# Kernel optimization log

Hardware: AMD Instinct MI355X
Metric: run time of the kernel (lower is better)

The kernel has to match this reference:

```python
import jax, jax.numpy as jnp
import numpy as np

S, B, NS, NC = 128, 64, 128, 8
D, Z, H, HI, NF = 32, 64, 128, 128, 2
N = NS * B
LOG2PI = float(np.log(2.0 * np.pi))
_m_in = np.arange(1, Z + 1)
_m_hid = (np.arange(HI) % (Z - 1)) + 1
MASK1 = jnp.asarray((_m_hid[None, :] >= _m_in[:, None]).astype(np.float32))  # [Z,HI]
MASK2 = jnp.asarray((_m_in[None, :] > _m_hid[:, None]).astype(np.float32))   # [HI,Z]


def setup_inputs() -> dict:
    key = jax.random.key(0)
    ks = jax.random.split(key, 16)
    r = lambda i, shape: jax.random.normal(ks[i], shape, jnp.float32) * 0.1
    return dict(
        input=jax.random.normal(ks[0], (S, B, D), jnp.float32),
        eps=jax.random.normal(ks[1], (S, N, Z), jnp.float32),
        u=jax.random.uniform(ks[2], (S, 3, NC, NS, B), dtype=jnp.float32),
        Wxh=r(3, (D, H)), Wzh=r(4, (Z, H)), bh=jnp.zeros(H, jnp.float32),
        Wg=r(5, (H, Z)), bg=jnp.zeros(Z, jnp.float32),
        Wp=r(6, (H, Z)), bp=jnp.zeros(Z, jnp.float32),
        Wz=r(7, (Z, Z)), bz=jnp.zeros(Z, jnp.float32),
        Wsc=r(8, (Z, Z)), bsc=jnp.zeros(Z, jnp.float32),
        iaf_W1=r(9, (NF, Z, HI)), iaf_b1=jnp.zeros((NF, HI), jnp.float32),
        iaf_Wm=r(10, (NF, HI, Z)), iaf_bm=jnp.zeros((NF, Z), jnp.float32),
        iaf_Ws=r(11, (NF, HI, Z)), iaf_bs=jnp.zeros((NF, Z), jnp.float32),
        We1=r(12, (Z, H)), be1=jnp.zeros(H, jnp.float32),
        We2=r(13, (H, 4 * NC)), be2=jnp.zeros(4 * NC, jnp.float32),
    )


def _forward(input, eps, u, Wxh, Wzh, bh, Wg, bg, Wp, bp, Wz, bz, Wsc, bsc,
             iaf_W1, iaf_b1, iaf_Wm, iaf_bm, iaf_Ws, iaf_bs, We1, be1, We2, be2):
    def step(z_prev, inp):
        x, eps_t, u_t = inp                        # x:[B,D] eps_t:[N,Z] u_t:[3,NC,NS,B]
        xr = jnp.tile(x, (NS, 1))                  # == input[i].repeat(n_samples, 1) -> [N,D]
        # GatedTransition
        h = jax.nn.relu(xr @ Wxh + z_prev @ Wzh + bh)
        gate = jax.nn.sigmoid(h @ Wg + bg)
        prop = h @ Wp + bp
        loc = (1.0 - gate) * (z_prev @ Wz + bz) + gate * prop
        scale = jax.nn.softplus(jax.nn.relu(prop) @ Wsc + bsc) + 1e-3
        # base rsample + log_prob of base sample (eps form)
        z = loc + scale * eps_t
        base_lp = jnp.sum(-0.5 * eps_t * eps_t - jnp.log(scale) - 0.5 * LOG2PI, axis=-1)
        # IAF stack: y = sigma*x + (1-sigma)*mu, cached log_prob = base_lp - sum log sigma
        logdet = jnp.zeros((N,), z.dtype)
        for f in range(NF):
            hh = jax.nn.relu(z @ (iaf_W1[f] * MASK1) + iaf_b1[f])
            mu = hh @ (iaf_Wm[f] * MASK2) + iaf_bm[f]
            sg = jax.nn.sigmoid(hh @ (iaf_Ws[f] * MASK2) + iaf_bs[f] + 1.0)
            z = sg * z + (1.0 - sg) * mu
            logdet = logdet + jnp.sum(jnp.log(sg), axis=-1)
        z_lp = (base_lp - logdet).reshape(NS, B)
        # Emitter -> [N, 4*NC]; .t().view(4,NC,NS,B).split([3,1])
        e = jax.nn.relu(z @ We1 + be1) @ We2 + be2
        et = e.T.reshape(4, NC, NS, B)
        logits, frac = et[:3], jax.nn.sigmoid(et[3:4])
        samp = (u_t < jax.nn.sigmoid(logits)).astype(jnp.float32)  # Bernoulli sample
        x_lp = samp * jax.nn.log_sigmoid(logits) + (1.0 - samp) * jax.nn.log_sigmoid(-logits)
        return z, (samp, frac, x_lp, z_lp)

    z0 = jnp.zeros((N, Z), input.dtype)
    _, (samples, fractions, x_logprobs, z_logprobs) = jax.lax.scan(step, z0, (input, eps, u))
    return samples, fractions, x_logprobs, z_logprobs


def reference(input, eps, u, Wxh, Wzh, bh, Wg, bg, Wp, bp, Wz, bz, Wsc, bsc,
              iaf_W1, iaf_b1, iaf_Wm, iaf_bm, iaf_Ws, iaf_bs, We1, be1, We2, be2):
    return _forward(input, eps, u, Wxh, Wzh, bh, Wg, bg, Wp, bp, Wz, bz, Wsc, bsc,
                    iaf_W1, iaf_b1, iaf_Wm, iaf_bm, iaf_Ws, iaf_bs, We1, be1, We2, be2)
```

## Files before the change

### kernel.cpp

```cpp
#include <hip/hip_runtime.h>


typedef _Float16 f16x8 __attribute__((ext_vector_type(8)));
typedef _Float16 f16x4 __attribute__((ext_vector_type(4)));
typedef float    f32x4 __attribute__((ext_vector_type(4)));
typedef unsigned short u16;

#define MFMA16(a,b,c) __builtin_amdgcn_mfma_f32_16x16x32_f16((a),(b),(c),0,0,0)

namespace {
constexpr int S = 128;
constexpr long FRAC_OFF = 25165824L;
constexpr long XLP_OFF  = 33554432L;
constexpr long ZLP_OFF  = 58720256L;
constexpr float HLOG2PI = 0.91893853320467274f;
constexpr float INVLO   = 1.0f / 2048.0f;

constexpr int C1HI = 0,      C1LO = 12288;
constexpr int GPHI = 24576,  GPLO = 40960;
constexpr int WZHI = 57344,  WZLO = 61440;
constexpr int SCHI = 65536,  SCLO = 69632;
constexpr int W1B  = 73728;
constexpr int MSB  = 106496;
constexpr int E1HI = 172032, E1LO = 180224;
constexpr int E2HI = 188416, E2LO = 192512;
constexpr int XHI  = 196608, XLO  = 458752;
}

__device__ __forceinline__ float sigm(float x)      { return 1.0f / (1.0f + __expf(-x)); }
__device__ __forceinline__ float softplusf_(float x){ return fmaxf(x, 0.f) + __logf(1.f + __expf(-fabsf(x))); }
__device__ __forceinline__ float logsigm(float x)   { return fminf(x, 0.f) - __logf(1.f + __expf(-fabsf(x))); }

__device__ __forceinline__ void split2(float v, _Float16& hi, _Float16& lo) {
    hi = (_Float16)v;
    lo = (_Float16)((v - (float)hi) * 2048.0f);
}

__device__ __forceinline__ f16x8 rdA(const u16* t, int row, int k, int strideEls, int swm) {
    int byte = ((row * strideEls + k) * 2) ^ ((row & swm) << 4);
    return *(const f16x8*)((const char*)t + byte);
}
__device__ __forceinline__ f16x8 ldB(const u16* wa, int base, int col, int K, int koff) {
    return *(const f16x8*)(wa + base + col * K + koff);
}

template<int NKS, int STRIDE, int SWM>
__device__ __forceinline__ void mmDual(const u16* Th, const u16* Tl, int lnc, int kf,
                                       const f16x8 (&wh)[NKS], const f16x8 (&wl)[NKS],
                                       float bias, f32x4& H0, f32x4& L0, f32x4& H1, f32x4& L1)
{
    H0 = (f32x4){bias, bias, bias, bias}; H1 = H0;
    L0 = (f32x4){0.f, 0.f, 0.f, 0.f};     L1 = L0;
#pragma unroll
    for (int ks = 0; ks < NKS; ++ks) {
        int k = ks * 32 + kf;
        f16x8 a0h = rdA(Th, lnc,      k, STRIDE, SWM);
        f16x8 a0l = rdA(Tl, lnc,      k, STRIDE, SWM);
        f16x8 a1h = rdA(Th, 16 + lnc, k, STRIDE, SWM);
        f16x8 a1l = rdA(Tl, 16 + lnc, k, STRIDE, SWM);
        H0 = MFMA16(a0h, wh[ks], H0); L0 = MFMA16(a0h, wl[ks], L0); L0 = MFMA16(a0l, wh[ks], L0);
        H1 = MFMA16(a1h, wh[ks], H1); L1 = MFMA16(a1h, wl[ks], L1); L1 = MFMA16(a1l, wh[ks], L1);
    }
}

template<bool RELU>
__device__ __forceinline__ void stAct(f32x4 H, f32x4 L, int rt, int lng, int col,
                                      u16* th, u16* tl, int strideEls, int swm)
{
#pragma unroll
    for (int q = 0; q < 4; ++q) {
        int row = rt * 16 + lng * 4 + q;
        float v = H[q] + L[q] * INVLO;
        if (RELU) v = fmaxf(v, 0.f);
        _Float16 hi, lo; split2(v, hi, lo);
        int byte = ((row * strideEls + col) * 2) ^ ((row & swm) << 4);
        *(_Float16*)((char*)th + byte) = hi;
        *(_Float16*)((char*)tl + byte) = lo;
    }
}
__device__ __forceinline__ void stScr(f32x4 H, f32x4 L, int rt, int lng, int col,
                                      float* s, int strideEls)
{
#pragma unroll
    for (int q = 0; q < 4; ++q) {
        int row = rt * 16 + lng * 4 + q;
        int byte = ((row * strideEls + col) * 4) ^ ((row & 7) << 4);
        *(float*)((char*)s + byte) = H[q] + L[q] * INVLO;
    }
}
__device__ __forceinline__ f32x4 rdS4(const float* s, int strideEls, int row, int c) {
    int byte = ((row * strideEls + c) * 4) ^ ((row & 7) << 4);
    return *(const f32x4*)((const char*)s + byte);
}
__device__ __forceinline__ float rdS1(const float* s, int strideEls, int row, int c) {
    int byte = ((row * strideEls + c) * 4) ^ ((row & 7) << 4);
    return *(const float*)((const char*)s + byte);
}
__device__ __forceinline__ void wrS4(float* s, int strideEls, int row, int c, f32x4 v) {
    int byte = ((row * strideEls + c) * 4) ^ ((row & 7) << 4);
    *(f32x4*)((char*)s + byte) = v;
}
__device__ __forceinline__ void wrF16x4(u16* t, int strideEls, int row, int c, f16x4 v) {
    int byte = ((row * strideEls + c) * 2) ^ ((row & 7) << 4);
    *(f16x4*)((char*)t + byte) = v;
}
__device__ __forceinline__ f16x4 rdF16x4(const u16* t, int strideEls, int row, int c) {
    int byte = ((row * strideEls + c) * 2) ^ ((row & 7) << 4);
    return *(const f16x4*)((const char*)t + byte);
}

__global__ void prep_kernel(const float* __restrict__ input,
                            const float* __restrict__ Wxh, const float* __restrict__ Wzh,
                            const float* __restrict__ Wg,  const float* __restrict__ Wp,
                            const float* __restrict__ Wz,  const float* __restrict__ Wsc,
                            const float* __restrict__ W1,  const float* __restrict__ Wm,
                            const float* __restrict__ Ws_, const float* __restrict__ We1,
                            const float* __restrict__ We2, u16* __restrict__ wa)
{
    int idx = blockIdx.x * 256 + threadIdx.x;
    if (idx < 98304) {
        int hio = 0, loo = 0; float v = 0.f;
        int i = idx;
        if (i < 12288) {
            int col = i / 96, k = i % 96;
            v = (k < 32) ? Wxh[k * 128 + col] : Wzh[(k - 32) * 128 + col];
            hio = C1HI + i; loo = C1LO + i;
        } else if (i < 28672) { int j = i - 12288;
            int col = j >> 7, k = j & 127;
            v = (col < 64) ? Wg[k * 64 + col] : Wp[k * 64 + col - 64];
            hio = GPHI + j; loo = GPLO + j;
        } else if (i < 32768) { int j = i - 28672;
            int col = j >> 6, k = j & 63; v = Wz[k * 64 + col];
            hio = WZHI + j; loo = WZLO + j;
        } else if (i < 36864) { int j = i - 32768;
            int col = j >> 6, k = j & 63; v = Wsc[k * 64 + col];
            hio = SCHI + j; loo = SCLO + j;
        } else if (i < 53248) { int j = i - 36864;
            int f = j >> 13, jj = j & 8191;
            int col = jj >> 6, k = jj & 63;
            v = W1[(f * 64 + k) * 128 + col] * (((col % 63) >= k) ? 1.f : 0.f);
            hio = W1B + f * 16384 + jj; loo = hio + 8192;
        } else if (i < 86016) { int j = i - 53248;
            int f = j >> 14, jj = j & 16383;
            int col = jj >> 7, k = jj & 127;
            if (col < 64) v = Wm[(f * 128 + k) * 64 + col] * (((k % 63) < col) ? 1.f : 0.f);
            else { int c = col - 64;
                   v = Ws_[(f * 128 + k) * 64 + c]         * (((k % 63) < c)   ? 1.f : 0.f); }
            hio = MSB + f * 32768 + jj; loo = hio + 16384;
        } else if (i < 94208) { int j = i - 86016;
            int col = j >> 6, k = j & 63; v = We1[k * 128 + col];
            hio = E1HI + j; loo = E1LO + j;
        } else { int j = i - 94208;
            int col = j >> 7, k = j & 127; v = We2[k * 32 + col];
            hio = E2HI + j; loo = E2LO + j;
        }
        _Float16 hi, lo; split2(v, hi, lo);
        wa[hio] = __builtin_bit_cast(u16, hi);
        wa[loo] = __builtin_bit_cast(u16, lo);
    } else {
        int j = idx - 98304;
        if (j < 262144) {
            float v = input[j];
            _Float16 hi, lo; split2(v, hi, lo);
            wa[XHI + j] = __builtin_bit_cast(u16, hi);
            wa[XLO + j] = __builtin_bit_cast(u16, lo);
        }
    }
}

__global__ __launch_bounds__(512, 2)
void ssm_mfma_kernel(const float* __restrict__ eps, const float* __restrict__ u,
                     const float* __restrict__ bh,  const float* __restrict__ bg,
                     const float* __restrict__ bp,  const float* __restrict__ bz,
                     const float* __restrict__ bsc, const float* __restrict__ b1,
                     const float* __restrict__ bm,  const float* __restrict__ bs,
                     const float* __restrict__ be1, const float* __restrict__ be2,
                     const u16* __restrict__ wa, float* __restrict__ out)
{
    __shared__ u16 tXh[32 * 32],  tXl[32 * 32];
    __shared__ u16 tZh[32 * 64],  tZl[32 * 64];
    __shared__ u16 tHh[32 * 128], tHl[32 * 128];
    __shared__ u16 tPh[32 * 64],  tPl[32 * 64];
    __shared__ float scrB[32 * 128];
    __shared__ float scrZ[32 * 64];
    __shared__ float scrL[32 * 64];
    __shared__ float lpS[32][16];

    const int tid = threadIdx.x;
    const int ln  = tid & 63, w = tid >> 6;
    const int lnc = ln & 15, lng = ln >> 4;
    const int r0  = blockIdx.x * 32, b0 = r0 & 63;
    const int kf  = lng * 8;
    const int col0  = w * 16 + lnc;
    const int colz  = (w & 3) * 16 + lnc;
    const int colE2 = (w & 1) * 16 + lnc;
    const int khE2  = w >> 1;
    const int crow  = tid >> 4, ccol4 = (tid & 15) * 4;
    const int erow  = tid & 31, c0 = (tid >> 5) * 2;

    f16x8 wC1h[3], wC1l[3], wGPh[4], wGPl[4], wZSh[2], wZSl[2];
    f16x8 wW1h[2][2], wW1l[2][2], wMSh[2][4], wMSl[2][4];
    f16x8 wE1h[2], wE1l[2], wE2h[1], wE2l[1];
#pragma unroll
    for (int ks = 0; ks < 3; ++ks) {
        wC1h[ks] = ldB(wa, C1HI, col0, 96, ks * 32 + kf);
        wC1l[ks] = ldB(wa, C1LO, col0, 96, ks * 32 + kf);
    }
#pragma unroll
    for (int ks = 0; ks < 4; ++ks) {
        wGPh[ks] = ldB(wa, GPHI, col0, 128, ks * 32 + kf);
        wGPl[ks] = ldB(wa, GPLO, col0, 128, ks * 32 + kf);
    }
    if (w < 4) {
#pragma unroll
        for (int ks = 0; ks < 2; ++ks) {
            wZSh[ks] = ldB(wa, WZHI, colz, 64, ks * 32 + kf);
            wZSl[ks] = ldB(wa, WZLO, colz, 64, ks * 32 + kf);
        }
    } else {
#pragma unroll
        for (int ks = 0; ks < 2; ++ks) {
            wZSh[ks] = ldB(wa, SCHI, colz, 64, ks * 32 + kf);
            wZSl[ks] = ldB(wa, SCLO, colz, 64, ks * 32 + kf);
        }
    }
#pragma unroll
    for (int f = 0; f < 2; ++f) {
#pragma unroll
        for (int ks = 0; ks < 2; ++ks) {
            wW1h[f][ks] = ldB(wa, W1B + f * 16384,        col0, 64, ks * 32 + kf);
            wW1l[f][ks] = ldB(wa, W1B + f * 16384 + 8192, col0, 64, ks * 32 + kf);
        }
#pragma unroll
        for (int ks = 0; ks < 4; ++ks) {
            wMSh[f][ks] = ldB(wa, MSB + f * 32768,         col0, 128, ks * 32 + kf);
            wMSl[f][ks] = ldB(wa, MSB + f * 32768 + 16384, col0, 128, ks * 32 + kf);
        }
    }
#pragma unroll
    for (int ks = 0; ks < 2; ++ks) {
        wE1h[ks] = ldB(wa, E1HI, col0, 64, ks * 32 + kf);
        wE1l[ks] = ldB(wa, E1LO, col0, 64, ks * 32 + kf);
    }
    wE2h[0] = ldB(wa, E2HI, colE2, 128, khE2 * 32 + kf);
    wE2l[0] = ldB(wa, E2LO, colE2, 128, khE2 * 32 + kf);

    const float bhv  = bh[col0];
    const float bGPv = (col0 < 64) ? bg[col0] : bp[col0 - 64];
    const float bzsv = (w < 4) ? bz[colz] : bsc[colz];
    float bW1v[2], bMSv[2];
#pragma unroll
    for (int f = 0; f < 2; ++f) {
        bW1v[f] = b1[f * 128 + col0];
        bMSv[f] = (col0 < 64) ? bm[f * 64 + col0] : bs[f * 64 + col0 - 64];
    }
    const float bE1v = be1[col0];
    const float bE2v = (khE2 == 0) ? be2[colE2] : 0.f;

    for (int i = tid; i < 32 * 64; i += 512) { tZh[i] = 0; tZl[i] = 0; }
    {
        int rr = tid >> 4, d2 = (tid & 15) * 2;
        int ge = (b0 + rr) * 32 + d2;
        unsigned xh = *(const unsigned*)(wa + XHI + ge);
        unsigned xl = *(const unsigned*)(wa + XLO + ge);
        int byte = (rr * 64 + d2 * 2) ^ ((rr & 3) << 4);
        *(unsigned*)((char*)tXh + byte) = xh;
        *(unsigned*)((char*)tXl + byte) = xl;
    }
    __syncthreads();

    for (int t = 0; t < S; ++t) {
        f32x4 epsv = *(const f32x4*)(eps + ((size_t)t * 8192 + r0 + crow) * 64 + ccol4);

        {
            f32x4 H0 = {bhv, bhv, bhv, bhv}, H1 = H0;
            f32x4 L0 = {0.f, 0.f, 0.f, 0.f}, L1 = L0;
            {
                f16x8 a0h = rdA(tXh, lnc, kf, 32, 3),      a0l = rdA(tXl, lnc, kf, 32, 3);
                f16x8 a1h = rdA(tXh, 16 + lnc, kf, 32, 3), a1l = rdA(tXl, 16 + lnc, kf, 32, 3);
                H0 = MFMA16(a0h, wC1h[0], H0); L0 = MFMA16(a0h, wC1l[0], L0); L0 = MFMA16(a0l, wC1h[0], L0);
                H1 = MFMA16(a1h, wC1h[0], H1); L1 = MFMA16(a1h, wC1l[0], L1); L1 = MFMA16(a1l, wC1h[0], L1);
            }
#pragma unroll
            for (int ks = 1; ks < 3; ++ks) {
                int k = (ks - 1) * 32 + kf;
                f16x8 a0h = rdA(tZh, lnc, k, 64, 7),      a0l = rdA(tZl, lnc, k, 64, 7);
                f16x8 a1h = rdA(tZh, 16 + lnc, k, 64, 7), a1l = rdA(tZl, 16 + lnc, k, 64, 7);
                H0 = MFMA16(a0h, wC1h[ks], H0); L0 = MFMA16(a0h, wC1l[ks], L0); L0 = MFMA16(a0l, wC1h[ks], L0);
                H1 = MFMA16(a1h, wC1h[ks], H1); L1 = MFMA16(a1h, wC1l[ks], L1); L1 = MFMA16(a1l, wC1h[ks], L1);
            }
            stAct<true>(H0, L0, 0, lng, col0, tHh, tHl, 128, 7);
            stAct<true>(H1, L1, 1, lng, col0, tHh, tHl, 128, 7);
        }
        if (w < 4) {
            f32x4 H0, L0, H1, L1;
            mmDual<2, 64, 7>(tZh, tZl, lnc, kf, wZSh, wZSl, bzsv, H0, L0, H1, L1);
            stScr(H0, L0, 0, lng, colz, scrZ, 64);
            stScr(H1, L1, 1, lng, colz, scrZ, 64);
        }
        __syncthreads();

        {
            f32x4 H0, L0, H1, L1;
            mmDual<4, 128, 7>(tHh, tHl, lnc, kf, wGPh, wGPl, bGPv, H0, L0, H1, L1);
            stScr(H0, L0, 0, lng, col0, scrB, 128);
            stScr(H1, L1, 1, lng, col0, scrB, 128);
        }
        __syncthreads();

        {
            f32x4 gp4 = rdS4(scrB, 128, crow, ccol4);
            f32x4 pr4 = rdS4(scrB, 128, crow, 64 + ccol4);
            f32x4 zw4 = rdS4(scrZ, 64, crow, ccol4);
            f32x4 loc4; f16x4 ph4, pl4;
#pragma unroll
            for (int i = 0; i < 4; ++i) {
                float g = sigm(gp4[i]);
                loc4[i] = (1.f - g) * zw4[i] + g * pr4[i];
                float rp = fmaxf(pr4[i], 0.f);
                _Float16 hi, lo; split2(rp, hi, lo); ph4[i] = hi; pl4[i] = lo;
            }
            wrS4(scrL, 64, crow, ccol4, loc4);
            wrF16x4(tPh, 64, crow, ccol4, ph4);
            wrF16x4(tPl, 64, crow, ccol4, pl4);
        }
        __syncthreads();

        if (w >= 4) {
            f32x4 H0, L0, H1, L1;
            mmDual<2, 64, 7>(tPh, tPl, lnc, kf, wZSh, wZSl, bzsv, H0, L0, H1, L1);
            stScr(H0, L0, 0, lng, colz, scrB, 128);
            stScr(H1, L1, 1, lng, colz, scrB, 128);
        }
        __syncthreads();

        float lp = 0.f;
        {
            f32x4 s4   = rdS4(scrB, 128, crow, ccol4);
            f32x4 loc4 = rdS4(scrL, 64, crow, ccol4);
            f16x4 zh4, zl4;
#pragma unroll
            for (int i = 0; i < 4; ++i) {
                float sc = softplusf_(s4[i]) + 0.001f;
                float zv = loc4[i] + sc * epsv[i];
                lp += -0.5f * epsv[i] * epsv[i] - __logf(sc) - HLOG2PI;
                _Float16 hi, lo; split2(zv, hi, lo); zh4[i] = hi; zl4[i] = lo;
            }
            wrF16x4(tZh, 64, crow, ccol4, zh4);
            wrF16x4(tZl, 64, crow, ccol4, zl4);
        }
        __syncthreads();

#pragma unroll
        for (int f = 0; f < 2; ++f) {
            {
                f32x4 H0, L0, H1, L1;
                mmDual<2, 64, 7>(tZh, tZl, lnc, kf, wW1h[f], wW1l[f], bW1v[f], H0, L0, H1, L1);
                stAct<true>(H0, L0, 0, lng, col0, tHh, tHl, 128, 7);
                stAct<true>(H1, L1, 1, lng, col0, tHh, tHl, 128, 7);
            }
            __syncthreads();
            {
                f32x4 H0, L0, H1, L1;
                mmDual<4, 128, 7>(tHh, tHl, lnc, kf, wMSh[f], wMSl[f], bMSv[f], H0, L0, H1, L1);
                stScr(H0, L0, 0, lng, col0, scrB, 128);
                stScr(H1, L1, 1, lng, col0, scrB, 128);
            }
            __syncthreads();
            {
                f32x4 mu4 = rdS4(scrB, 128, crow, ccol4);
                f32x4 sp4 = rdS4(scrB, 128, crow, 64 + ccol4);
                f16x4 zh4 = rdF16x4(tZh, 64, crow, ccol4);
                f16x4 zl4 = rdF16x4(tZl, 64, crow, ccol4);
                f16x4 nzh, nzl;
#pragma unroll
                for (int i = 0; i < 4; ++i) {
                    float zv = (float)zh4[i] + (float)zl4[i] * INVLO;
                    float sg = sigm(sp4[i] + 1.0f);
                    float zn = sg * zv + (1.f - sg) * mu4[i];
                    lp -= __logf(sg);
                    _Float16 hi, lo; split2(zn, hi, lo); nzh[i] = hi; nzl[i] = lo;
                }
                wrF16x4(tZh, 64, crow, ccol4, nzh);
                wrF16x4(tZl, 64, crow, ccol4, nzl);
                if (f == 1) lpS[crow][tid & 15] = lp;
            }
            __syncthreads();
        }

        float uv0 = 0.f, uv1 = 0.f;
        if (c0 < 24) {
            uv0 = u[((size_t)((t * 3 + (c0 >> 3)) * 8 + (c0 & 7))) * 8192 + r0 + erow];
            int c1 = c0 + 1;
            uv1 = u[((size_t)((t * 3 + (c1 >> 3)) * 8 + (c1 & 7))) * 8192 + r0 + erow];
        }
        {
            f32x4 H0, L0, H1, L1;
            mmDual<2, 64, 7>(tZh, tZl, lnc, kf, wE1h, wE1l, bE1v, H0, L0, H1, L1);
            stAct<true>(H0, L0, 0, lng, col0, tHh, tHl, 128, 7);
            stAct<true>(H1, L1, 1, lng, col0, tHh, tHl, 128, 7);
        }
        __syncthreads();

        {
            f32x4 H0, L0, H1, L1;
            H0 = (f32x4){bE2v, bE2v, bE2v, bE2v}; H1 = H0;
            L0 = (f32x4){0.f, 0.f, 0.f, 0.f};     L1 = L0;
            int k = khE2 * 32 + kf;
            f16x8 a0h = rdA(tHh, lnc, k, 128, 7),      a0l = rdA(tHl, lnc, k, 128, 7);
            f16x8 a1h = rdA(tHh, 16 + lnc, k, 128, 7), a1l = rdA(tHl, 16 + lnc, k, 128, 7);
            H0 = MFMA16(a0h, wE2h[0], H0); L0 = MFMA16(a0h, wE2l[0], L0); L0 = MFMA16(a0l, wE2h[0], L0);
            H1 = MFMA16(a1h, wE2h[0], H1); L1 = MFMA16(a1h, wE2l[0], L1); L1 = MFMA16(a1l, wE2h[0], L1);
            stScr(H0, L0, 0, lng, khE2 * 32 + colE2, scrB, 128);
            stScr(H1, L1, 1, lng, khE2 * 32 + colE2, scrB, 128);
        }
        if (t + 1 < S) {
            int rr = tid >> 4, d2 = (tid & 15) * 2;
            int ge = ((t + 1) * 64 + b0 + rr) * 32 + d2;
            unsigned xh = *(const unsigned*)(wa + XHI + ge);
            unsigned xl = *(const unsigned*)(wa + XLO + ge);
            int byte = (rr * 64 + d2 * 2) ^ ((rr & 3) << 4);
            *(unsigned*)((char*)tXh + byte) = xh;
            *(unsigned*)((char*)tXl + byte) = xl;
        }
        __syncthreads();

        {
#pragma unroll
            for (int q = 0; q < 2; ++q) {
                int col = c0 + q;
                float v = 0.f;
#pragma unroll
                for (int kh = 0; kh < 4; ++kh) v += rdS1(scrB, 128, erow, kh * 32 + col);
                if (col < 24) {
                    long plane = ((long)(t * 3 + (col >> 3)) * 8 + (col & 7)) * 8192 + r0 + erow;
                    float sg = sigm(v);
                    bool hit = ((q == 0) ? uv0 : uv1) < sg;
                    out[plane] = hit ? 1.f : 0.f;
                    out[XLP_OFF + plane] = hit ? logsigm(v) : logsigm(-v);
                } else {
                    long pf = ((long)t * 8 + (col & 7)) * 8192 + r0 + erow;
                    out[FRAC_OFF + pf] = sigm(v);
                }
            }
            if (tid < 32) {
                float s = 0.f;
#pragma unroll
                for (int g2 = 0; g2 < 16; ++g2) s += lpS[tid][g2];
                out[ZLP_OFF + (long)t * 8192 + r0 + tid] = s;
            }
        }
    }
}

extern "C" void kernel_launch(void* const* d_in, const int* in_sizes, int n_in,
                              void* d_out, int out_size, void* d_ws, size_t ws_size,
                              hipStream_t stream)
{
    const float* input = (const float*)d_in[0];
    const float* eps   = (const float*)d_in[1];
    const float* u     = (const float*)d_in[2];
    const float* Wxh   = (const float*)d_in[3];
    const float* Wzh   = (const float*)d_in[4];
    const float* bh    = (const float*)d_in[5];
    const float* Wg    = (const float*)d_in[6];
    const float* bg    = (const float*)d_in[7];
    const float* Wp    = (const float*)d_in[8];
    const float* bp    = (const float*)d_in[9];
    const float* Wz    = (const float*)d_in[10];
    const float* bz    = (const float*)d_in[11];
    const float* Wsc   = (const float*)d_in[12];
    const float* bsc   = (const float*)d_in[13];
    const float* W1    = (const float*)d_in[14];
    const float* b1    = (const float*)d_in[15];
    const float* Wm    = (const float*)d_in[16];
    const float* bm    = (const float*)d_in[17];
    const float* Ws    = (const float*)d_in[18];
    const float* bs    = (const float*)d_in[19];
    const float* We1   = (const float*)d_in[20];
    const float* be1   = (const float*)d_in[21];
    const float* We2   = (const float*)d_in[22];
    const float* be2   = (const float*)d_in[23];

    u16* wa = (u16*)d_ws;

    hipLaunchKernelGGL(prep_kernel, dim3(1408), dim3(256), 0, stream,
                       input, Wxh, Wzh, Wg, Wp, Wz, Wsc, W1, Wm, Ws, We1, We2, wa);

    hipLaunchKernelGGL(ssm_mfma_kernel, dim3(256), dim3(512), 0, stream,
                       eps, u, bh, bg, bp, bz, bsc, b1, bm, bs, be1, be2,
                       wa, (float*)d_out);
}
```

Baseline: 2.960 ms.

## Stage low-part MADE and emitter weights in LDS to cut register pressure

Moves the low-precision residual fragments of the IAF mean/scale weights and the first emitter layer from per-thread registers into swizzled shared memory loaded once at kernel start. The matmuls now read those B fragments from LDS each step. The separate loc scratch buffer is folded into the unused half of the shared scratch. This reduces VGPR pressure and spilling, but adds about 80KB of LDS per block, which may limit blocks per CU, and adds LDS reads to the inner loop.

```diff
diff --git a/kernel.cpp b/kernel.cpp
--- a/kernel.cpp
+++ b/kernel.cpp
@@ -42,6 +42,10 @@
 }
 __device__ __forceinline__ f16x8 ldB(const u16* wa, int base, int col, int K, int koff) {
     return *(const f16x8*)(wa + base + col * K + koff);
+}
+__device__ __forceinline__ f16x8 ldLo(const u16* lds, int el, int col) {
+    int byte = (el * 2) ^ ((col & 7) << 4);
+    return *(const f16x8*)((const char*)lds + byte);
 }
 
 template<int NKS, int STRIDE, int SWM>
@@ -183,8 +187,9 @@
     __shared__ u16 tPh[32 * 64],  tPl[32 * 64];
     __shared__ float scrB[32 * 128];
     __shared__ float scrZ[32 * 64];
-    __shared__ float scrL[32 * 64];
     __shared__ float lpS[32][16];
+    __shared__ u16 loMS[32768];
+    __shared__ u16 loE1[8192];
 
     const int tid = threadIdx.x;
     const int ln  = tid & 63, w = tid >> 6;
@@ -198,9 +203,24 @@
     const int crow  = tid >> 4, ccol4 = (tid & 15) * 4;
     const int erow  = tid & 31, c0 = (tid >> 5) * 2;
 
+    for (int i8 = tid; i8 < 4096; i8 += 512) {
+        int el = i8 * 8;
+        int f = el >> 14, rem = el & 16383, col = rem >> 7;
+        f16x8 v = *(const f16x8*)(wa + MSB + f * 32768 + 16384 + rem);
+        int byte = (el * 2) ^ ((col & 7) << 4);
+        *(f16x8*)((char*)loMS + byte) = v;
+    }
+    for (int i8 = tid; i8 < 1024; i8 += 512) {
+        int el = i8 * 8;
+        int col = el >> 6;
+        f16x8 v = *(const f16x8*)(wa + E1LO + el);
+        int byte = (el * 2) ^ ((col & 7) << 4);
+        *(f16x8*)((char*)loE1 + byte) = v;
+    }
+
     f16x8 wC1h[3], wC1l[3], wGPh[4], wGPl[4], wZSh[2], wZSl[2];
-    f16x8 wW1h[2][2], wW1l[2][2], wMSh[2][4], wMSl[2][4];
-    f16x8 wE1h[2], wE1l[2], wE2h[1], wE2l[1];
+    f16x8 wW1h[2][2], wW1l[2][2], wMSh[2][4];
+    f16x8 wE1h[2], wE2h[1], wE2l[1];
 #pragma unroll
     for (int ks = 0; ks < 3; ++ks) {
         wC1h[ks] = ldB(wa, C1HI, col0, 96, ks * 32 + kf);
@@ -233,14 +253,12 @@
         }
 #pragma unroll
         for (int ks = 0; ks < 4; ++ks) {
-            wMSh[f][ks] = ldB(wa, MSB + f * 32768,         col0, 128, ks * 32 + kf);
-            wMSl[f][ks] = ldB(wa, MSB + f * 32768 + 16384, col0, 128, ks * 32 + kf);
+            wMSh[f][ks] = ldB(wa, MSB + f * 32768, col0, 128, ks * 32 + kf);
         }
     }
 #pragma unroll
     for (int ks = 0; ks < 2; ++ks) {
         wE1h[ks] = ldB(wa, E1HI, col0, 64, ks * 32 + kf);
-        wE1l[ks] = ldB(wa, E1LO, col0, 64, ks * 32 + kf);
     }
     wE2h[0] = ldB(wa, E2HI, colE2, 128, khE2 * 32 + kf);
     wE2l[0] = ldB(wa, E2LO, colE2, 128, khE2 * 32 + kf);
@@ -320,7 +338,7 @@
                 float rp = fmaxf(pr4[i], 0.f);
                 _Float16 hi, lo; split2(rp, hi, lo); ph4[i] = hi; pl4[i] = lo;
             }
-            wrS4(scrL, 64, crow, ccol4, loc4);
+            wrS4(scrB, 128, crow, 64 + ccol4, loc4);
             wrF16x4(tPh, 64, crow, ccol4, ph4);
             wrF16x4(tPl, 64, crow, ccol4, pl4);
         }
@@ -337,7 +355,7 @@
         float lp = 0.f;
         {
             f32x4 s4   = rdS4(scrB, 128, crow, ccol4);
-            f32x4 loc4 = rdS4(scrL, 64, crow, ccol4);
+            f32x4 loc4 = rdS4(scrB, 128, crow, 64 + ccol4);
             f16x4 zh4, zl4;
 #pragma unroll
             for (int i = 0; i < 4; ++i) {
@@ -361,8 +379,18 @@
             }
             __syncthreads();
             {
-                f32x4 H0, L0, H1, L1;
-                mmDual<4, 128, 7>(tHh, tHl, lnc, kf, wMSh[f], wMSl[f], bMSv[f], H0, L0, H1, L1);
+                f32x4 H0 = {bMSv[f], bMSv[f], bMSv[f], bMSv[f]}, H1 = H0;
+                f32x4 L0 = {0.f, 0.f, 0.f, 0.f}, L1 = L0;
+#pragma unroll
+                for (int ks = 0; ks < 4; ++ks) {
+                    int k = ks * 32 + kf;
+                    f16x8 a0h = rdA(tHh, lnc, k, 128, 7),      a0l = rdA(tHl, lnc, k, 128, 7);
+                    f16x8 a1h = rdA(tHh, 16 + lnc, k, 128, 7), a1l = rdA(tHl, 16 + lnc, k, 128, 7);
+                    f16x8 bhf = wMSh[f][ks];
+                    f16x8 blf = ldLo(loMS, f * 16384 + col0 * 128 + k, col0);
+                    H0 = MFMA16(a0h, bhf, H0); L0 = MFMA16(a0h, blf, L0); L0 = MFMA16(a0l, bhf, L0);
+                    H1 = MFMA16(a1h, bhf, H1); L1 = MFMA16(a1h, blf, L1); L1 = MFMA16(a1l, bhf, L1);
+                }
                 stScr(H0, L0, 0, lng, col0, scrB, 128);
                 stScr(H1, L1, 1, lng, col0, scrB, 128);
             }
@@ -395,8 +423,18 @@
             uv1 = u[((size_t)((t * 3 + (c1 >> 3)) * 8 + (c1 & 7))) * 8192 + r0 + erow];
         }
         {
-            f32x4 H0, L0, H1, L1;
-            mmDual<2, 64, 7>(tZh, tZl, lnc, kf, wE1h, wE1l, bE1v, H0, L0, H1, L1);
+            f32x4 H0 = {bE1v, bE1v, bE1v, bE1v}, H1 = H0;
+            f32x4 L0 = {0.f, 0.f, 0.f, 0.f}, L1 = L0;
+#pragma unroll
+            for (int ks = 0; ks < 2; ++ks) {
+                int k = ks * 32 + kf;
+                f16x8 a0h = rdA(tZh, lnc, k, 64, 7),      a0l = rdA(tZl, lnc, k, 64, 7);
+                f16x8 a1h = rdA(tZh, 16 + lnc, k, 64, 7), a1l = rdA(tZl, 16 + lnc, k, 64, 7);
+                f16x8 bhf = wE1h[ks];
+                f16x8 blf = ldLo(loE1, col0 * 64 + k, col0);
+                H0 = MFMA16(a0h, bhf, H0); L0 = MFMA16(a0h, blf, L0); L0 = MFMA16(a0l, bhf, L0);
+                H1 = MFMA16(a1h, bhf, H1); L1 = MFMA16(a1h, blf, L1); L1 = MFMA16(a1l, bhf, L1);
+            }
             stAct<true>(H0, L0, 0, lng, col0, tHh, tHl, 128, 7);
             stAct<true>(H1, L1, 1, lng, col0, tHh, tHl, 128, 7);
         }
```

Result: slower. 3.026 ms (+2.2%).
